# Kernel tuning notes

Hardware: AMD Instinct MI355X
Metric: run time of the kernel (lower is better)

The kernel has to match this reference:

```python
import jax, jax.numpy as jnp
import numpy as np

B, N, M = 8, 8192, 2048
C, CP = 256, 256          # num_features, num_features_prev
D1, D2 = 256, 256         # layer_dims
BN_EPS = 1e-5


def setup_inputs() -> dict:
    key = jax.random.key(0)
    ks = jax.random.split(key, 8)
    return {
        "xyz": jax.random.normal(ks[0], (B, N, 3), dtype=jnp.float32),
        "xyz_prev": jax.random.normal(ks[1], (B, M, 3), dtype=jnp.float32),
        "features": jax.random.normal(ks[2], (B, C, N), dtype=jnp.float32),
        "features_prev": jax.random.normal(ks[3], (B, CP, M), dtype=jnp.float32),
        "w1": jax.random.normal(ks[4], (D1, C + CP), dtype=jnp.float32) * 0.02,
        "b1": jnp.zeros((D1,), dtype=jnp.float32),
        "g1": jnp.ones((D1,), dtype=jnp.float32),
        "beta1": jnp.zeros((D1,), dtype=jnp.float32),
        "w2": jax.random.normal(ks[5], (D2, D1), dtype=jnp.float32) * 0.02,
        "b2": jnp.zeros((D2,), dtype=jnp.float32),
        "g2": jnp.ones((D2,), dtype=jnp.float32),
        "beta2": jnp.zeros((D2,), dtype=jnp.float32),
    }


def _three_nn(unknown, known):
    # squared pairwise distances via GEMM form: [B, n, m]
    sq_u = jnp.sum(unknown * unknown, axis=-1)          # [B, n]
    sq_k = jnp.sum(known * known, axis=-1)              # [B, m]
    d2 = sq_u[:, :, None] + sq_k[:, None, :] - 2.0 * jnp.einsum(
        "bnd,bmd->bnm", unknown, known)
    neg_top, idx = jax.lax.top_k(-d2, 3)                # 3 smallest, ascending
    dist = jnp.sqrt(jnp.maximum(-neg_top, 0.0))         # [B, n, 3]
    return dist, idx


def _three_interpolate(features, idx, weight):
    # features [B, c, m], idx [B, n, 3], weight [B, n, 3] -> [B, c, n]
    gathered = jax.vmap(lambda f, i: f[:, i])(features, idx)  # [B, c, n, 3]
    return jnp.einsum("bcnk,bnk->bcn", gathered, weight)


def _bn_relu(x, gamma, beta):
    # training-mode BatchNorm1d over (batch, points), biased variance
    mean = jnp.mean(x, axis=(0, 2), keepdims=True)
    var = jnp.var(x, axis=(0, 2), keepdims=True)
    xh = (x - mean) * jax.lax.rsqrt(var + BN_EPS)
    return jnp.maximum(xh * gamma[None, :, None] + beta[None, :, None], 0.0)


def reference(xyz, xyz_prev, features, features_prev,
              w1, b1, g1, beta1, w2, b2, g2, beta2):
    dist, idx = _three_nn(xyz, xyz_prev)
    inv = 1.0 / (dist + 1e-8)
    weights = inv / jnp.sum(inv, axis=2, keepdims=True)           # [B, n, 3]
    new_features = _three_interpolate(features_prev, idx, weights)  # [B, cp, n]
    x = jnp.concatenate([new_features, features], axis=1)           # [B, cp+c, n]
    x = _bn_relu(jnp.einsum("oi,bin->bon", w1, x) + b1[None, :, None], g1, beta1)
    x = _bn_relu(jnp.einsum("oi,bin->bon", w2, x) + b2[None, :, None], g2, beta2)
    return x
```

## Files before the change

kernel.cpp:

```cpp
#include <hip/hip_runtime.h>

#define BDIM 8
#define NPTS 8192
#define MPTS 2048
#define NCHUNK 8
#define CHSZ 256
#define NSAMP 65536.0f
#define PITCH 40

typedef __attribute__((ext_vector_type(8))) short bf16x8;
typedef __attribute__((ext_vector_type(4))) float f32x4;

static __device__ __forceinline__ unsigned short f2bf(float f) {
  unsigned int x = __float_as_uint(f);
  x += 0x7FFFu + ((x >> 16) & 1u);
  return (unsigned short)(x >> 16);
}
static __device__ __forceinline__ float bf2f(unsigned short u) {
  return __uint_as_float(((unsigned int)u) << 16);
}

__global__ __launch_bounds__(256)
void three_nn_part_kernel(const float* __restrict__ xyz, const float* __restrict__ xyz_prev,
                          float4* __restrict__ pd, int4* __restrict__ pi) {
  __shared__ __align__(16) float4 pk[CHSZ];
  const int tid = threadIdx.x;
  const int ch = blockIdx.y, b = blockIdx.z;
  const int mbase = ch*CHSZ;
  {
    const int j = mbase + tid;
    float x = xyz_prev[((size_t)b*MPTS + j)*3 + 0];
    float y = xyz_prev[((size_t)b*MPTS + j)*3 + 1];
    float z = xyz_prev[((size_t)b*MPTS + j)*3 + 2];
    float s = __fadd_rn(__fadd_rn(__fmul_rn(x,x), __fmul_rn(y,y)), __fmul_rn(z,z));
    pk[tid] = make_float4(x, y, z, s);
  }
  __syncthreads();
  const int n = blockIdx.x*256 + tid;
  const size_t qoff = ((size_t)b*NPTS + n)*3;
  const float qx = xyz[qoff], qy = xyz[qoff+1], qz = xyz[qoff+2];
  const float squ = __fadd_rn(__fadd_rn(__fmul_rn(qx,qx), __fmul_rn(qy,qy)), __fmul_rn(qz,qz));

  float d0 = 3.4e38f, d1 = 3.4e38f, d2v = 3.4e38f;
  int j0 = 0, j1 = 0, j2 = 0;
  for (int m = 0; m < CHSZ; m += 16) {
    float dd[16];
    #pragma unroll
    for (int u = 0; u < 16; ++u) {
      const float4 p = pk[m + u];
      float dot = __fadd_rn(__fadd_rn(__fmul_rn(qx,p.x), __fmul_rn(qy,p.y)), __fmul_rn(qz,p.z));
      dd[u] = __fsub_rn(__fadd_rn(squ, p.w), __fmul_rn(2.0f, dot));
    }
    float mn = dd[0];
    #pragma unroll
    for (int u = 1; u < 16; ++u) mn = fminf(mn, dd[u]);
    if (mn < d2v) {
      #pragma unroll
      for (int u = 0; u < 16; ++u) {
        const float v = dd[u];
        if (v < d2v) {
          if (v < d1) {
            d2v = d1; j2 = j1;
            if (v < d0) { d1 = d0; j1 = j0; d0 = v; j0 = mbase + m + u; }
            else        { d1 = v;  j1 = mbase + m + u; }
          } else { d2v = v; j2 = mbase + m + u; }
        }
      }
    }
  }
  const size_t q = (size_t)b*NPTS + n;
  pd[(size_t)ch*(BDIM*NPTS) + q] = make_float4(d0, d1, d2v, 0.f);
  pi[(size_t)ch*(BDIM*NPTS) + q] = make_int4(j0, j1, j2, 0);
}

__global__ __launch_bounds__(256)
void nn_merge_kernel(const float4* __restrict__ pd, const int4* __restrict__ pi,
                     int* __restrict__ idx_out, float* __restrict__ wgt_out) {
  const size_t q = (size_t)blockIdx.x*256 + threadIdx.x;
  float d0 = 3.4e38f, d1 = 3.4e38f, d2v = 3.4e38f;
  int j0 = 0, j1 = 0, j2 = 0;
  #pragma unroll
  for (int c = 0; c < NCHUNK; ++c) {
    const float4 dv = pd[(size_t)c*(BDIM*NPTS) + q];
    const int4   iv = pi[(size_t)c*(BDIM*NPTS) + q];
    const float dl[3] = {dv.x, dv.y, dv.z};
    const int   jl[3] = {iv.x, iv.y, iv.z};
    #pragma unroll
    for (int t = 0; t < 3; ++t) {
      const float v = dl[t]; const int j = jl[t];
      if (v < d2v) {
        if (v < d1) {
          d2v = d1; j2 = j1;
          if (v < d0) { d1 = d0; j1 = j0; d0 = v; j0 = j; }
          else        { d1 = v;  j1 = j; }
        } else { d2v = v; j2 = j; }
      }
    }
  }
  const float s0 = sqrtf(fmaxf(d0, 0.f));
  const float s1 = sqrtf(fmaxf(d1, 0.f));
  const float s2 = sqrtf(fmaxf(d2v, 0.f));
  const float i0 = 1.f/(s0 + 1e-8f), i1 = 1.f/(s1 + 1e-8f), i2 = 1.f/(s2 + 1e-8f);
  const float sum = i0 + i1 + i2;
  idx_out[q*3] = j0; idx_out[q*3+1] = j1; idx_out[q*3+2] = j2;
  wgt_out[q*3] = i0/sum; wgt_out[q*3+1] = i1/sum; wgt_out[q*3+2] = i2/sum;
}

__global__ __launch_bounds__(256)
void cvt2_kernel(const float* __restrict__ w1, const float* __restrict__ w2,
                 unsigned short* __restrict__ d1, unsigned short* __restrict__ d2) {
  int t = blockIdx.x*256 + threadIdx.x;
  if (t < 131072) d1[t] = f2bf(w1[t]);
  else            d2[t - 131072] = f2bf(w2[t - 131072]);
}

template<int SRCW, int DPITCH, int DOFF>
__global__ __launch_bounds__(256)
void trans_bf16_kernel(const float* __restrict__ src, unsigned short* __restrict__ dst) {
  __shared__ __align__(16) unsigned short St[64][72];
  const int tid = threadIdx.x;
  const int n0 = blockIdx.x*64, c0 = blockIdx.y*64, b = blockIdx.z;
  const int cl = tid >> 2;
  #pragma unroll
  for (int i = 0; i < 4; ++i) {
    int nl = (tid & 3)*16 + i*4;
    float4 v = *(const float4*)&src[((size_t)(b*256 + c0 + cl))*SRCW + n0 + nl];
    St[cl][nl]   = f2bf(v.x); St[cl][nl+1] = f2bf(v.y);
    St[cl][nl+2] = f2bf(v.z); St[cl][nl+3] = f2bf(v.w);
  }
  __syncthreads();
  #pragma unroll
  for (int i = 0; i < 2; ++i) {
    int u = tid + i*256;
    int nl = u >> 3, c8 = (u & 7)*8;
    unsigned short tmp[8];
    #pragma unroll
    for (int j = 0; j < 8; ++j) tmp[j] = St[c8 + j][nl];
    *(uint4*)&dst[((size_t)(b*SRCW + n0 + nl))*DPITCH + DOFF + c0 + c8] = *(uint4*)tmp;
  }
}

__global__ __launch_bounds__(512)
void gemm1_fused_kernel(const unsigned short* __restrict__ W,
                        const unsigned short* __restrict__ Xf,
                        const unsigned short* __restrict__ fpT,
                        const int* __restrict__ idx, const float* __restrict__ wgt,
                        const float* __restrict__ bias,
                        unsigned short* __restrict__ Y, float* __restrict__ part) {
  __shared__ __align__(16) unsigned short Ws[256*PITCH];
  __shared__ __align__(16) unsigned short Xs[128*PITCH];
  __shared__ float lsum[256], lsq[256];
  const int tid = threadIdx.x;
  const int b = blockIdx.y, n0 = blockIdx.x*128;
  const int row = tid >> 2, seg = tid & 3;

  if (tid < 256) { lsum[tid] = 0.f; lsq[tid] = 0.f; }

  const size_t p = ((size_t)b*NPTS + n0 + row)*3;
  const int   i0 = idx[p],  i1 = idx[p+1],  i2 = idx[p+2];
  const float w0 = wgt[p],  w1 = wgt[p+1],  w2 = wgt[p+2];
  const unsigned short* fb  = fpT + (size_t)b*MPTS*256;
  const unsigned short* Xfb = Xf  + ((size_t)(b*NPTS + n0) + row)*256;

  uint4 wv0 = *(const uint4*)&W[(size_t)row*512 + seg*8];
  uint4 wv1 = *(const uint4*)&W[(size_t)(row+128)*512 + seg*8];
  uint4 xv;
  {
    const int k0 = seg*8;
    uint4 a0 = *(const uint4*)&fb[(size_t)i0*256 + k0];
    uint4 a1 = *(const uint4*)&fb[(size_t)i1*256 + k0];
    uint4 a2 = *(const uint4*)&fb[(size_t)i2*256 + k0];
    const unsigned short* u0 = (const unsigned short*)&a0;
    const unsigned short* u1 = (const unsigned short*)&a1;
    const unsigned short* u2 = (const unsigned short*)&a2;
    unsigned short r[8];
    #pragma unroll
    for (int j = 0; j < 8; ++j)
      r[j] = f2bf(bf2f(u0[j])*w0 + bf2f(u1[j])*w1 + bf2f(u2[j])*w2);
    xv = *(uint4*)r;
  }

  f32x4 acc[4][4];
  #pragma unroll
  for (int i = 0; i < 4; ++i)
    #pragma unroll
    for (int j = 0; j < 4; ++j) acc[i][j] = (f32x4){0.f,0.f,0.f,0.f};

  const int lane = tid & 63, l16 = lane & 15, quad = lane >> 4;
  const int wave = tid >> 6, wo = wave >> 1, wn = wave & 1;

  for (int kt = 0; kt < 16; ++kt) {
    __syncthreads();
    *(uint4*)&Ws[row*PITCH + seg*8]       = wv0;
    *(uint4*)&Ws[(row+128)*PITCH + seg*8] = wv1;
    *(uint4*)&Xs[row*PITCH + seg*8]       = xv;
    __syncthreads();
    if (kt + 1 < 16) {
      const int k0 = (kt+1)*32;
      wv0 = *(const uint4*)&W[(size_t)row*512 + k0 + seg*8];
      wv1 = *(const uint4*)&W[(size_t)(row+128)*512 + k0 + seg*8];
      const int kx = k0 + seg*8;
      if (kx < 256) {
        uint4 a0 = *(const uint4*)&fb[(size_t)i0*256 + kx];
        uint4 a1 = *(const uint4*)&fb[(size_t)i1*256 + kx];
        uint4 a2 = *(const uint4*)&fb[(size_t)i2*256 + kx];
        const unsigned short* u0 = (const unsigned short*)&a0;
        const unsigned short* u1 = (const unsigned short*)&a1;
        const unsigned short* u2 = (const unsigned short*)&a2;
        unsigned short r[8];
        #pragma unroll
        for (int j = 0; j < 8; ++j)
          r[j] = f2bf(bf2f(u0[j])*w0 + bf2f(u1[j])*w1 + bf2f(u2[j])*w2);
        xv = *(uint4*)r;
      } else {
        xv = *(const uint4*)&Xfb[kx - 256];
      }
    }
    bf16x8 af[4], bfr[4];
    #pragma unroll
    for (int to = 0; to < 4; ++to)
      af[to] = *(const bf16x8*)&Ws[(wo*64 + to*16 + l16)*PITCH + quad*8];
    #pragma unroll
    for (int tn = 0; tn < 4; ++tn)
      bfr[tn] = *(const bf16x8*)&Xs[(wn*64 + tn*16 + l16)*PITCH + quad*8];
    #pragma unroll
    for (int to = 0; to < 4; ++to)
      #pragma unroll
      for (int tn = 0; tn < 4; ++tn)
        acc[to][tn] = __builtin_amdgcn_mfma_f32_16x16x32_bf16(af[to], bfr[tn], acc[to][tn], 0, 0, 0);
  }

  #pragma unroll
  for (int to = 0; to < 4; ++to) {
    #pragma unroll
    for (int r = 0; r < 4; ++r) {
      const int o = wo*64 + to*16 + quad*4 + r;
      const float bv = bias[o];
      float ps = 0.f, qs = 0.f;
      #pragma unroll
      for (int tn = 0; tn < 4; ++tn) {
        float v = acc[to][tn][r] + bv;
        acc[to][tn][r] = v;
        ps += v; qs = fmaf(v, v, qs);
      }
      #pragma unroll
      for (int m = 1; m < 16; m <<= 1) { ps += __shfl_xor(ps, m); qs += __shfl_xor(qs, m); }
      if (l16 == 0) { atomicAdd(&lsum[o], ps); atomicAdd(&lsq[o], qs); }
    }
  }
  #pragma unroll
  for (int to = 0; to < 4; ++to)
    #pragma unroll
    for (int tn = 0; tn < 4; ++tn) {
      const int n = n0 + wn*64 + tn*16 + l16;
      const int o = wo*64 + to*16 + quad*4;
      unsigned int lo = (unsigned)f2bf(acc[to][tn][0]) | ((unsigned)f2bf(acc[to][tn][1]) << 16);
      unsigned int hi = (unsigned)f2bf(acc[to][tn][2]) | ((unsigned)f2bf(acc[to][tn][3]) << 16);
      *(uint2*)&Y[((size_t)(b*NPTS + n))*256 + o] = make_uint2(lo, hi);
    }
  __syncthreads();
  if (tid < 256) {
    const int blk = b*gridDim.x + blockIdx.x;
    part[(size_t)blk*512 + tid]       = lsum[tid];
    part[(size_t)blk*512 + 256 + tid] = lsq[tid];
  }
}

template<int KD, int MODE>
__global__ __launch_bounds__(512)
void gemm_t_kernel(const unsigned short* __restrict__ W, const unsigned short* __restrict__ X,
                   const float* __restrict__ bias, const float* __restrict__ scl,
                   const float* __restrict__ shf, unsigned short* __restrict__ Y,
                   float* __restrict__ part) {
  __shared__ __align__(16) unsigned short Ws[256*PITCH];
  __shared__ __align__(16) unsigned short Xs[128*PITCH];
  __shared__ float lsum[256], lsq[256];
  const int tid = threadIdx.x;
  const int b = blockIdx.y, n0 = blockIdx.x*128;
  const int row = tid >> 2, seg = tid & 3;
  const unsigned short* Xb = X + (size_t)(b*NPTS + n0)*KD;

  if (tid < 256) { lsum[tid] = 0.f; lsq[tid] = 0.f; }

  uint4 wv0 = *(const uint4*)&W[(size_t)row*KD + seg*8];
  uint4 wv1 = *(const uint4*)&W[(size_t)(row+128)*KD + seg*8];
  uint4 xv  = *(const uint4*)&Xb[(size_t)row*KD + seg*8];

  f32x4 acc[4][4];
  #pragma unroll
  for (int i = 0; i < 4; ++i)
    #pragma unroll
    for (int j = 0; j < 4; ++j) acc[i][j] = (f32x4){0.f,0.f,0.f,0.f};

  const int lane = tid & 63, l16 = lane & 15, quad = lane >> 4;
  const int wave = tid >> 6, wo = wave >> 1, wn = wave & 1;

  for (int kt = 0; kt < KD/32; ++kt) {
    __syncthreads();
    *(uint4*)&Ws[row*PITCH + seg*8]       = wv0;
    *(uint4*)&Ws[(row+128)*PITCH + seg*8] = wv1;
    if (MODE == 0) {
      *(uint4*)&Xs[row*PITCH + seg*8] = xv;
    } else {
      const int kc = kt*32 + seg*8;
      float4 s0 = *(const float4*)&scl[kc], s1 = *(const float4*)&scl[kc+4];
      float4 h0 = *(const float4*)&shf[kc], h1 = *(const float4*)&shf[kc+4];
      const unsigned short* xu = (const unsigned short*)&xv;
      unsigned short t[8];
      t[0] = f2bf(fmaxf(fmaf(bf2f(xu[0]), s0.x, h0.x), 0.f));
      t[1] = f2bf(fmaxf(fmaf(bf2f(xu[1]), s0.y, h0.y), 0.f));
      t[2] = f2bf(fmaxf(fmaf(bf2f(xu[2]), s0.z, h0.z), 0.f));
      t[3] = f2bf(fmaxf(fmaf(bf2f(xu[3]), s0.w, h0.w), 0.f));
      t[4] = f2bf(fmaxf(fmaf(bf2f(xu[4]), s1.x, h1.x), 0.f));
      t[5] = f2bf(fmaxf(fmaf(bf2f(xu[5]), s1.y, h1.y), 0.f));
      t[6] = f2bf(fmaxf(fmaf(bf2f(xu[6]), s1.z, h1.z), 0.f));
      t[7] = f2bf(fmaxf(fmaf(bf2f(xu[7]), s1.w, h1.w), 0.f));
      *(uint4*)&Xs[row*PITCH + seg*8] = *(uint4*)t;
    }
    __syncthreads();
    if (kt + 1 < KD/32) {
      const int k0 = (kt+1)*32;
      wv0 = *(const uint4*)&W[(size_t)row*KD + k0 + seg*8];
      wv1 = *(const uint4*)&W[(size_t)(row+128)*KD + k0 + seg*8];
      xv  = *(const uint4*)&Xb[(size_t)row*KD + k0 + seg*8];
    }
    bf16x8 af[4], bfr[4];
    #pragma unroll
    for (int to = 0; to < 4; ++to)
      af[to] = *(const bf16x8*)&Ws[(wo*64 + to*16 + l16)*PITCH + quad*8];
    #pragma unroll
    for (int tn = 0; tn < 4; ++tn)
      bfr[tn] = *(const bf16x8*)&Xs[(wn*64 + tn*16 + l16)*PITCH + quad*8];
    #pragma unroll
    for (int to = 0; to < 4; ++to)
      #pragma unroll
      for (int tn = 0; tn < 4; ++tn)
        acc[to][tn] = __builtin_amdgcn_mfma_f32_16x16x32_bf16(af[to], bfr[tn], acc[to][tn], 0, 0, 0);
  }

  #pragma unroll
  for (int to = 0; to < 4; ++to) {
    #pragma unroll
    for (int r = 0; r < 4; ++r) {
      const int o = wo*64 + to*16 + quad*4 + r;
      const float bv = bias[o];
      float p = 0.f, q = 0.f;
      #pragma unroll
      for (int tn = 0; tn < 4; ++tn) {
        float v = acc[to][tn][r] + bv;
        acc[to][tn][r] = v;
        p += v; q = fmaf(v, v, q);
      }
      #pragma unroll
      for (int m = 1; m < 16; m <<= 1) { p += __shfl_xor(p, m); q += __shfl_xor(q, m); }
      if (l16 == 0) { atomicAdd(&lsum[o], p); atomicAdd(&lsq[o], q); }
    }
  }
  #pragma unroll
  for (int to = 0; to < 4; ++to)
    #pragma unroll
    for (int tn = 0; tn < 4; ++tn) {
      const int n = n0 + wn*64 + tn*16 + l16;
      const int o = wo*64 + to*16 + quad*4;
      unsigned int lo = (unsigned)f2bf(acc[to][tn][0]) | ((unsigned)f2bf(acc[to][tn][1]) << 16);
      unsigned int hi = (unsigned)f2bf(acc[to][tn][2]) | ((unsigned)f2bf(acc[to][tn][3]) << 16);
      *(uint2*)&Y[((size_t)(b*NPTS + n))*256 + o] = make_uint2(lo, hi);
    }
  __syncthreads();
  if (tid < 256) {
    const int blk = b*gridDim.x + blockIdx.x;
    part[(size_t)blk*512 + tid]       = lsum[tid];
    part[(size_t)blk*512 + 256 + tid] = lsq[tid];
  }
}

__global__ __launch_bounds__(256)
void bn_reduce_kernel(const float* __restrict__ part, const float* __restrict__ g,
                      const float* __restrict__ beta, float* __restrict__ scl,
                      float* __restrict__ shf) {
  __shared__ float ls[4], lq[4];
  const int o = blockIdx.x;
  const int t = threadIdx.x;
  float s = part[(size_t)t*512 + o]        + part[(size_t)(t+256)*512 + o];
  float q = part[(size_t)t*512 + 256 + o]  + part[(size_t)(t+256)*512 + 256 + o];
  #pragma unroll
  for (int m = 1; m < 64; m <<= 1) { s += __shfl_xor(s, m); q += __shfl_xor(q, m); }
  const int w = t >> 6;
  if ((t & 63) == 0) { ls[w] = s; lq[w] = q; }
  __syncthreads();
  if (t == 0) {
    const float ss = ls[0] + ls[1] + ls[2] + ls[3];
    const float qq = lq[0] + lq[1] + lq[2] + lq[3];
    const float inv_n = 1.0f / NSAMP;
    const float mean = ss * inv_n;
    const float var  = qq * inv_n - mean*mean;
    const float sc = g[o] * rsqrtf(var + 1e-5f);
    scl[o] = sc;
    shf[o] = beta[o] - mean * sc;
  }
}

__global__ __launch_bounds__(256)
void bn2_t_kernel(const unsigned short* __restrict__ Yt, const float* __restrict__ scl,
                  const float* __restrict__ shf, float* __restrict__ out) {
  __shared__ __align__(16) unsigned short T[64][72];
  const int tid = threadIdx.x;
  const int n0 = blockIdx.x*64, o0 = blockIdx.y*64, b = blockIdx.z;
  #pragma unroll
  for (int i = 0; i < 2; ++i) {
    int u = tid + i*256;
    int nl = u >> 3, o8 = (u & 7)*8;
    uint4 v = *(const uint4*)&Yt[((size_t)(b*NPTS + n0 + nl))*256 + o0 + o8];
    *(uint4*)&T[nl][o8] = v;
  }
  __syncthreads();
  #pragma unroll
  for (int i = 0; i < 4; ++i) {
    int u = tid + i*256;
    int ol = u >> 4, n4 = (u & 15)*4;
    const float s = scl[o0+ol], h = shf[o0+ol];
    float4 v;
    v.x = fmaxf(fmaf(bf2f(T[n4  ][ol]), s, h), 0.f);
    v.y = fmaxf(fmaf(bf2f(T[n4+1][ol]), s, h), 0.f);
    v.z = fmaxf(fmaf(bf2f(T[n4+2][ol]), s, h), 0.f);
    v.w = fmaxf(fmaf(bf2f(T[n4+3][ol]), s, h), 0.f);
    *(float4*)&out[((size_t)(b*256 + o0 + ol))*NPTS + n0 + n4] = v;
  }
}

extern "C" void kernel_launch(void* const* d_in, const int* in_sizes, int n_in,
                              void* d_out, int out_size, void* d_ws, size_t ws_size,
                              hipStream_t stream) {
  const float* xyz           = (const float*)d_in[0];
  const float* xyz_prev      = (const float*)d_in[1];
  const float* features      = (const float*)d_in[2];
  const float* features_prev = (const float*)d_in[3];
  const float* w1    = (const float*)d_in[4];
  const float* b1    = (const float*)d_in[5];
  const float* g1    = (const float*)d_in[6];
  const float* beta1 = (const float*)d_in[7];
  const float* w2    = (const float*)d_in[8];
  const float* b2    = (const float*)d_in[9];
  const float* g2    = (const float*)d_in[10];
  const float* beta2 = (const float*)d_in[11];
  float* out = (float*)d_out;

  char* ws = (char*)d_ws;
  int*            idxb = (int*)ws;
  float*          wgtb = (float*)(ws + 786432);
  float*          bn   = (float*)(ws + 1572864);
  unsigned short* w1b  = (unsigned short*)(ws + 1581056);
  unsigned short* w2b  = (unsigned short*)(ws + 1843200);
  unsigned short* Xf   = (unsigned short*)(ws + 2097152);
  unsigned short* y2t  = Xf;
  unsigned short* y1t  = (unsigned short*)d_out;
  unsigned short* fpT  = (unsigned short*)((char*)d_out + 33554432);
  float*          part = (float*)((char*)d_out + 41943040);
  float4*         pd   = (float4*)((char*)d_out + 46137344);
  int4*           pi   = (int4*)((char*)d_out + 54525952);

  float* bn1_scl = bn;        float* bn1_shf = bn + 256;
  float* bn2_scl = bn + 512;  float* bn2_shf = bn + 768;

  cvt2_kernel<<<768, 256, 0, stream>>>(w1, w2, w1b, w2b);

  three_nn_part_kernel<<<dim3(NPTS/256, NCHUNK, BDIM), 256, 0, stream>>>(xyz, xyz_prev, pd, pi);
  nn_merge_kernel<<<(BDIM*NPTS)/256, 256, 0, stream>>>(pd, pi, idxb, wgtb);

  trans_bf16_kernel<NPTS, 256, 0><<<dim3(NPTS/64, 4, BDIM), 256, 0, stream>>>(features, Xf);
  trans_bf16_kernel<MPTS, 256, 0><<<dim3(MPTS/64, 4, BDIM), 256, 0, stream>>>(features_prev, fpT);

  gemm1_fused_kernel<<<dim3(NPTS/128, BDIM), 512, 0, stream>>>(
      w1b, Xf, fpT, idxb, wgtb, b1, y1t, part);
  bn_reduce_kernel<<<256, 256, 0, stream>>>(part, g1, beta1, bn1_scl, bn1_shf);

  gemm_t_kernel<256, 1><<<dim3(NPTS/128, BDIM), 512, 0, stream>>>(
      w2b, y1t, b2, bn1_scl, bn1_shf, y2t, part);
  bn_reduce_kernel<<<256, 256, 0, stream>>>(part, g2, beta2, bn2_scl, bn2_shf);

  bn2_t_kernel<<<dim3(NPTS/64, 4, BDIM), 256, 0, stream>>>(y2t, bn2_scl, bn2_shf, out);
}
```

Before: 305.8 us.

## Merge three-NN, feature transposes and weight casts into one heterogeneous prep kernel

Replaces four independent launches (weight bf16 cast, partial three-NN, and two feature transposes) with a single kernel whose blocks are split by slot into compute-bound NN blocks and memory-bound transpose and cast blocks. Interleaving them in groups of 31 lets ALU-heavy distance work overlap with bandwidth-heavy transposes on the same CUs and removes launch gaps. Costs are a larger kernel with branch-dependent register pressure: the launch bounds ask for 8 blocks per CU, and the shared-memory buffer is sized for the largest role.

```diff
diff --git a/kernel.cpp b/kernel.cpp
--- a/kernel.cpp
+++ b/kernel.cpp
@@ -20,57 +20,119 @@
   return __uint_as_float(((unsigned int)u) << 16);
 }
 
-__global__ __launch_bounds__(256)
-void three_nn_part_kernel(const float* __restrict__ xyz, const float* __restrict__ xyz_prev,
-                          float4* __restrict__ pd, int4* __restrict__ pi) {
-  __shared__ __align__(16) float4 pk[CHSZ];
+__global__ __launch_bounds__(256, 8)
+void prep_kernel(const float* __restrict__ xyz, const float* __restrict__ xyz_prev,
+                 float4* __restrict__ pd, int4* __restrict__ pi,
+                 const float* __restrict__ features, unsigned short* __restrict__ Xf,
+                 const float* __restrict__ features_prev, unsigned short* __restrict__ fpT,
+                 const float* __restrict__ w1, const float* __restrict__ w2,
+                 unsigned short* __restrict__ w1b, unsigned short* __restrict__ w2b) {
+  __shared__ __align__(16) char smem[9216];
   const int tid = threadIdx.x;
-  const int ch = blockIdx.y, b = blockIdx.z;
-  const int mbase = ch*CHSZ;
-  {
-    const int j = mbase + tid;
-    float x = xyz_prev[((size_t)b*MPTS + j)*3 + 0];
-    float y = xyz_prev[((size_t)b*MPTS + j)*3 + 1];
-    float z = xyz_prev[((size_t)b*MPTS + j)*3 + 2];
-    float s = __fadd_rn(__fadd_rn(__fmul_rn(x,x), __fmul_rn(y,y)), __fmul_rn(z,z));
-    pk[tid] = make_float4(x, y, z, s);
-  }
-  __syncthreads();
-  const int n = blockIdx.x*256 + tid;
-  const size_t qoff = ((size_t)b*NPTS + n)*3;
-  const float qx = xyz[qoff], qy = xyz[qoff+1], qz = xyz[qoff+2];
-  const float squ = __fadd_rn(__fadd_rn(__fmul_rn(qx,qx), __fmul_rn(qy,qy)), __fmul_rn(qz,qz));
-
-  float d0 = 3.4e38f, d1 = 3.4e38f, d2v = 3.4e38f;
-  int j0 = 0, j1 = 0, j2 = 0;
-  for (int m = 0; m < CHSZ; m += 16) {
-    float dd[16];
-    #pragma unroll
-    for (int u = 0; u < 16; ++u) {
-      const float4 p = pk[m + u];
-      float dot = __fadd_rn(__fadd_rn(__fmul_rn(qx,p.x), __fmul_rn(qy,p.y)), __fmul_rn(qz,p.z));
-      dd[u] = __fsub_rn(__fadd_rn(squ, p.w), __fmul_rn(2.0f, dot));
-    }
-    float mn = dd[0];
-    #pragma unroll
-    for (int u = 1; u < 16; ++u) mn = fminf(mn, dd[u]);
-    if (mn < d2v) {
+  const int grp = blockIdx.x / 31, slot = blockIdx.x % 31;
+
+  if (slot < 8) {
+    const int id = grp*8 + slot;
+    float4* pk = (float4*)smem;
+    const int ch = (id >> 5) & 7, b = id >> 8;
+    const int mbase = ch*CHSZ;
+    {
+      const int j = mbase + tid;
+      float x = xyz_prev[((size_t)b*MPTS + j)*3 + 0];
+      float y = xyz_prev[((size_t)b*MPTS + j)*3 + 1];
+      float z = xyz_prev[((size_t)b*MPTS + j)*3 + 2];
+      float s = __fadd_rn(__fadd_rn(__fmul_rn(x,x), __fmul_rn(y,y)), __fmul_rn(z,z));
+      pk[tid] = make_float4(x, y, z, s);
+    }
+    __syncthreads();
+    const int n = (id & 31)*256 + tid;
+    const size_t qoff = ((size_t)b*NPTS + n)*3;
+    const float qx = xyz[qoff], qy = xyz[qoff+1], qz = xyz[qoff+2];
+    const float squ = __fadd_rn(__fadd_rn(__fmul_rn(qx,qx), __fmul_rn(qy,qy)), __fmul_rn(qz,qz));
+
+    float d0 = 3.4e38f, d1 = 3.4e38f, d2v = 3.4e38f;
+    int j0 = 0, j1 = 0, j2 = 0;
+    for (int m = 0; m < CHSZ; m += 16) {
+      float dd[16];
       #pragma unroll
       for (int u = 0; u < 16; ++u) {
-        const float v = dd[u];
-        if (v < d2v) {
-          if (v < d1) {
-            d2v = d1; j2 = j1;
-            if (v < d0) { d1 = d0; j1 = j0; d0 = v; j0 = mbase + m + u; }
-            else        { d1 = v;  j1 = mbase + m + u; }
-          } else { d2v = v; j2 = mbase + m + u; }
+        const float4 p = pk[m + u];
+        float dot = __fadd_rn(__fadd_rn(__fmul_rn(qx,p.x), __fmul_rn(qy,p.y)), __fmul_rn(qz,p.z));
+        dd[u] = __fsub_rn(__fadd_rn(squ, p.w), __fmul_rn(2.0f, dot));
+      }
+      float mn = dd[0];
+      #pragma unroll
+      for (int u = 1; u < 16; ++u) mn = fminf(mn, dd[u]);
+      if (mn < d2v) {
+        #pragma unroll
+        for (int u = 0; u < 16; ++u) {
+          const float v = dd[u];
+          if (v < d2v) {
+            if (v < d1) {
+              d2v = d1; j2 = j1;
+              if (v < d0) { d1 = d0; j1 = j0; d0 = v; j0 = mbase + m + u; }
+              else        { d1 = v;  j1 = mbase + m + u; }
+            } else { d2v = v; j2 = mbase + m + u; }
+          }
         }
       }
     }
-  }
-  const size_t q = (size_t)b*NPTS + n;
-  pd[(size_t)ch*(BDIM*NPTS) + q] = make_float4(d0, d1, d2v, 0.f);
-  pi[(size_t)ch*(BDIM*NPTS) + q] = make_int4(j0, j1, j2, 0);
+    const size_t q = (size_t)b*NPTS + n;
+    pd[(size_t)ch*(BDIM*NPTS) + q] = make_float4(d0, d1, d2v, 0.f);
+    pi[(size_t)ch*(BDIM*NPTS) + q] = make_int4(j0, j1, j2, 0);
+
+  } else if (slot < 24) {
+    const int id = grp*16 + (slot - 8);
+    unsigned short (*St)[72] = (unsigned short(*)[72])smem;
+    const int n0 = (id & 127)*64, c0 = ((id >> 7) & 3)*64, b = id >> 9;
+    const int cl = tid >> 2;
+    #pragma unroll
+    for (int i = 0; i < 4; ++i) {
+      int nl = (tid & 3)*16 + i*4;
+      float4 v = *(const float4*)&features[((size_t)(b*256 + c0 + cl))*NPTS + n0 + nl];
+      St[cl][nl]   = f2bf(v.x); St[cl][nl+1] = f2bf(v.y);
+      St[cl][nl+2] = f2bf(v.z); St[cl][nl+3] = f2bf(v.w);
+    }
+    __syncthreads();
+    #pragma unroll
+    for (int i = 0; i < 2; ++i) {
+      int u = tid + i*256;
+      int nl = u >> 3, c8 = (u & 7)*8;
+      unsigned short tmp[8];
+      #pragma unroll
+      for (int j = 0; j < 8; ++j) tmp[j] = St[c8 + j][nl];
+      *(uint4*)&Xf[((size_t)(b*NPTS + n0 + nl))*256 + c0 + c8] = *(uint4*)tmp;
+    }
+
+  } else if (slot < 28) {
+    const int id = grp*4 + (slot - 24);
+    unsigned short (*St)[72] = (unsigned short(*)[72])smem;
+    const int n0 = (id & 31)*64, c0 = ((id >> 5) & 3)*64, b = id >> 7;
+    const int cl = tid >> 2;
+    #pragma unroll
+    for (int i = 0; i < 4; ++i) {
+      int nl = (tid & 3)*16 + i*4;
+      float4 v = *(const float4*)&features_prev[((size_t)(b*256 + c0 + cl))*MPTS + n0 + nl];
+      St[cl][nl]   = f2bf(v.x); St[cl][nl+1] = f2bf(v.y);
+      St[cl][nl+2] = f2bf(v.z); St[cl][nl+3] = f2bf(v.w);
+    }
+    __syncthreads();
+    #pragma unroll
+    for (int i = 0; i < 2; ++i) {
+      int u = tid + i*256;
+      int nl = u >> 3, c8 = (u & 7)*8;
+      unsigned short tmp[8];
+      #pragma unroll
+      for (int j = 0; j < 8; ++j) tmp[j] = St[c8 + j][nl];
+      *(uint4*)&fpT[((size_t)(b*MPTS + n0 + nl))*256 + c0 + c8] = *(uint4*)tmp;
+    }
+
+  } else {
+    const int id = grp*3 + (slot - 28);
+    const int t = id*256 + tid;
+    if (t < 131072) w1b[t] = f2bf(w1[t]);
+    else            w2b[t - 131072] = f2bf(w2[t - 131072]);
+  }
 }
 
 __global__ __launch_bounds__(256)
@@ -104,40 +166,6 @@
   const float sum = i0 + i1 + i2;
   idx_out[q*3] = j0; idx_out[q*3+1] = j1; idx_out[q*3+2] = j2;
   wgt_out[q*3] = i0/sum; wgt_out[q*3+1] = i1/sum; wgt_out[q*3+2] = i2/sum;
-}
-
-__global__ __launch_bounds__(256)
-void cvt2_kernel(const float* __restrict__ w1, const float* __restrict__ w2,
-                 unsigned short* __restrict__ d1, unsigned short* __restrict__ d2) {
-  int t = blockIdx.x*256 + threadIdx.x;
-  if (t < 131072) d1[t] = f2bf(w1[t]);
-  else            d2[t - 131072] = f2bf(w2[t - 131072]);
-}
-
-template<int SRCW, int DPITCH, int DOFF>
-__global__ __launch_bounds__(256)
-void trans_bf16_kernel(const float* __restrict__ src, unsigned short* __restrict__ dst) {
-  __shared__ __align__(16) unsigned short St[64][72];
-  const int tid = threadIdx.x;
-  const int n0 = blockIdx.x*64, c0 = blockIdx.y*64, b = blockIdx.z;
-  const int cl = tid >> 2;
-  #pragma unroll
-  for (int i = 0; i < 4; ++i) {
-    int nl = (tid & 3)*16 + i*4;
-    float4 v = *(const float4*)&src[((size_t)(b*256 + c0 + cl))*SRCW + n0 + nl];
-    St[cl][nl]   = f2bf(v.x); St[cl][nl+1] = f2bf(v.y);
-    St[cl][nl+2] = f2bf(v.z); St[cl][nl+3] = f2bf(v.w);
-  }
-  __syncthreads();
-  #pragma unroll
-  for (int i = 0; i < 2; ++i) {
-    int u = tid + i*256;
-    int nl = u >> 3, c8 = (u & 7)*8;
-    unsigned short tmp[8];
-    #pragma unroll
-    for (int j = 0; j < 8; ++j) tmp[j] = St[c8 + j][nl];
-    *(uint4*)&dst[((size_t)(b*SRCW + n0 + nl))*DPITCH + DOFF + c0 + c8] = *(uint4*)tmp;
-  }
 }
 
 __global__ __launch_bounds__(512)
@@ -462,13 +490,10 @@
   float* bn1_scl = bn;        float* bn1_shf = bn + 256;
   float* bn2_scl = bn + 512;  float* bn2_shf = bn + 768;
 
-  cvt2_kernel<<<768, 256, 0, stream>>>(w1, w2, w1b, w2b);
-
-  three_nn_part_kernel<<<dim3(NPTS/256, NCHUNK, BDIM), 256, 0, stream>>>(xyz, xyz_prev, pd, pi);
+  prep_kernel<<<7936, 256, 0, stream>>>(xyz, xyz_prev, pd, pi,
+                                        features, Xf, features_prev, fpT,
+                                        w1, w2, w1b, w2b);
   nn_merge_kernel<<<(BDIM*NPTS)/256, 256, 0, stream>>>(pd, pi, idxb, wgtb);
-
-  trans_bf16_kernel<NPTS, 256, 0><<<dim3(NPTS/64, 4, BDIM), 256, 0, stream>>>(features, Xf);
-  trans_bf16_kernel<MPTS, 256, 0><<<dim3(MPTS/64, 4, BDIM), 256, 0, stream>>>(features_prev, fpT);
 
   gemm1_fused_kernel<<<dim3(NPTS/128, BDIM), 512, 0, stream>>>(
       w1b, Xf, fpT, idxb, wgtb, b1, y1t, part);
```

After: 285.4 us. 1.07x faster.
